# Kernel optimization log

Measured on AMD Instinct MI355X. Metric: run time of the kernel, lower is better.

## Reference

```python
import jax, jax.numpy as jnp
import numpy as np

B, IN, MEM, CTX, H = 8192, 1024, 1024, 1024, 4
DH = CTX // H

def setup_inputs() -> dict:
    key = jax.random.key(0)
    ks = jax.random.split(key, 20)
    s = 0.02
    d = {
        'input_tensor': jax.random.normal(ks[0], (B, IN), jnp.float32),
        'previous_memory': jax.random.normal(ks[1], (B, MEM), jnp.float32),
        # MultiheadAttention packed in_proj (q,k,v) and out_proj
        'in_proj_w': jax.random.normal(ks[2], (3 * CTX, CTX), jnp.float32) * s,
        'in_proj_b': jnp.zeros((3 * CTX,), jnp.float32),
        'out_proj_w': jax.random.normal(ks[3], (CTX, CTX), jnp.float32) * s,
        'out_proj_b': jnp.zeros((CTX,), jnp.float32),
        # input/memory projections
        'ip_w': jax.random.normal(ks[4], (CTX, IN), jnp.float32) * s,
        'ip_b': jnp.zeros((CTX,), jnp.float32),
        'mp_w': jax.random.normal(ks[5], (CTX, MEM), jnp.float32) * s,
        'mp_b': jnp.zeros((CTX,), jnp.float32),
        # forget / output gates
        'fg_w': jax.random.normal(ks[6], (MEM, MEM + IN), jnp.float32) * s,
        'fg_b': jnp.zeros((MEM,), jnp.float32),
        'og_w': jax.random.normal(ks[7], (MEM, MEM), jnp.float32) * s,
        'og_b': jnp.zeros((MEM,), jnp.float32),
        # GRUCell weights (PyTorch layout: [3*hidden, in], gates order r,z,n)
        'gru_w_ih': jax.random.normal(ks[8], (3 * MEM, CTX), jnp.float32) * s,
        'gru_b_ih': jnp.zeros((3 * MEM,), jnp.float32),
        'gru_w_hh': jax.random.normal(ks[9], (3 * MEM, MEM), jnp.float32) * s,
        'gru_b_hh': jnp.zeros((3 * MEM,), jnp.float32),
    }
    return d

def _forward(input_tensor, previous_memory, in_proj_w, in_proj_b, out_proj_w, out_proj_b,
             ip_w, ip_b, mp_w, mp_b, fg_w, fg_b, og_w, og_b,
             gru_w_ih, gru_b_ih, gru_w_hh, gru_b_hh):
    # projections
    pi = input_tensor @ ip_w.T + ip_b          # [B, CTX] (query; also context/value)
    pm = previous_memory @ mp_w.T + mp_b       # [B, CTX] (key)
    # MHA with q_len = kv_len = 1: softmax over a single key -> weights = 1
    wq, wk, wv = jnp.split(in_proj_w, 3, axis=0)
    bq, bk, bv = jnp.split(in_proj_b, 3, axis=0)
    q = (pi @ wq.T + bq).reshape(B, H, DH)
    k = (pm @ wk.T + bk).reshape(B, H, DH)
    v = (pi @ wv.T + bv).reshape(B, H, DH)
    scores = jnp.sum(q * k, axis=-1, keepdims=True) / jnp.sqrt(jnp.float32(DH))  # [B,H,1]
    w = jax.nn.softmax(scores, axis=-1)        # all ones (single key)
    attn = (w * v).reshape(B, CTX)             # == v
    context_aware = attn @ out_proj_w.T + out_proj_b  # [B, CTX]
    attention_weights = jnp.mean(w, axis=1)[:, None, :]  # [B,1,1], avg over heads
    # forget gate
    forget_in = jnp.concatenate([previous_memory, input_tensor], axis=-1)
    fgate = jax.nn.sigmoid(forget_in @ fg_w.T + fg_b)
    gated_mem = previous_memory * fgate
    # GRUCell (PyTorch semantics)
    gi = context_aware @ gru_w_ih.T + gru_b_ih
    gh = gated_mem @ gru_w_hh.T + gru_b_hh
    gi_r, gi_z, gi_n = jnp.split(gi, 3, axis=-1)
    gh_r, gh_z, gh_n = jnp.split(gh, 3, axis=-1)
    r = jax.nn.sigmoid(gi_r + gh_r)
    z = jax.nn.sigmoid(gi_z + gh_z)
    n = jnp.tanh(gi_n + r * gh_n)
    updated = (1.0 - z) * n + z * gated_mem
    ogate = jax.nn.sigmoid(updated @ og_w.T + og_b)
    return updated * ogate, attention_weights

def reference(input_tensor, previous_memory, in_proj_w, in_proj_b, out_proj_w, out_proj_b,
              ip_w, ip_b, mp_w, mp_b, fg_w, fg_b, og_w, og_b,
              gru_w_ih, gru_b_ih, gru_w_hh, gru_b_hh):
    return _forward(input_tensor, previous_memory, in_proj_w, in_proj_b, out_proj_w, out_proj_b,
                    ip_w, ip_b, mp_w, mp_b, fg_w, fg_b, og_w, og_b,
                    gru_w_ih, gru_b_ih, gru_w_hh, gru_b_hh)
```

## Files before the change

### kernel.cpp

```cpp
#include <hip/hip_runtime.h>
#include <cstdint>
#include <cstddef>


typedef __bf16 bf16;
typedef bf16 bf16x4 __attribute__((ext_vector_type(4)));
typedef bf16 bf16x8 __attribute__((ext_vector_type(8)));
typedef float f32x4 __attribute__((ext_vector_type(4)));

#define B_ROWS 8192

__device__ __forceinline__ float sigmoid_f(float x) {
    return 1.0f / (1.0f + __expf(-x));
}
__device__ __forceinline__ float tanh_f(float x) {
    return 1.0f - 2.0f / (__expf(2.0f * x) + 1.0f);
}

template <int BM>
__device__ __forceinline__ void gemm_core_tb(
    bf16* sA, bf16* sB,
    const bf16* __restrict__ A, int lda,
    const bf16* __restrict__ W, int ldw,
    const float* __restrict__ bias,
    int N, int K, int brow, int bcol, int epi,
    bf16* __restrict__ out_bf, float* __restrict__ out_f32,
    const float* __restrict__ aux_f32, const bf16* __restrict__ aux_bf,
    int tld)
{
    constexpr int AI = BM / 32;
    const int tid  = threadIdx.x;
    const int lane = tid & 63;
    const int wave = tid >> 6;
    const int wr   = (wave & 1) * (BM / 2);
    const int wc   = (wave >> 1) * 64;
    const int lrow = lane & 15;
    const int lq   = lane >> 4;

    f32x4 acc[AI][4];
#pragma unroll
    for (int i = 0; i < AI; ++i)
#pragma unroll
        for (int j = 0; j < 4; ++j) {
            f32x4 z = {0.0f, 0.0f, 0.0f, 0.0f};
            acc[i][j] = z;
        }

    auto stage = [&](bf16* dA, bf16* dB, int k0) {
#pragma unroll
        for (int i = 0; i < BM / 64; ++i) {
            const int s   = tid + i * 256;
            const int row = s >> 2;
            const int col = (((s & 3) ^ ((s >> 3) & 3)) << 3);
            const bf16* gp = A + (size_t)(brow + row) * lda + (k0 + col);
            __builtin_amdgcn_global_load_lds(
                (const __attribute__((address_space(1))) void*)gp,
                (__attribute__((address_space(3))) void*)(&dA[s * 8]),
                16, 0, 0);
        }
#pragma unroll
        for (int i = 0; i < 2; ++i) {
            const int s   = tid + i * 256;
            const int row = s >> 2;
            const int col = (((s & 3) ^ ((s >> 3) & 3)) << 3);
            const bf16* gp = W + (size_t)(bcol + row) * ldw + (k0 + col);
            __builtin_amdgcn_global_load_lds(
                (const __attribute__((address_space(1))) void*)gp,
                (__attribute__((address_space(3))) void*)(&dB[s * 8]),
                16, 0, 0);
        }
    };

#define WAIT_LPS()                                                   \
    do {                                                             \
        if constexpr (BM == 128)                                     \
            asm volatile("s_waitcnt vmcnt(4)" ::: "memory");         \
        else                                                         \
            asm volatile("s_waitcnt vmcnt(3)" ::: "memory");         \
    } while (0)

    const int NT = K >> 5;

    bf16* a0 = sA;               bf16* b0 = sB;
    bf16* a1 = sA + BM * 32;     bf16* b1 = sB + 4096;
    bf16* a2 = sA + 2 * BM * 32; bf16* b2 = sB + 2 * 4096;

    stage(a0, b0, 0);
    stage(a1, b1, NT > 1 ? 32 : 0);
    WAIT_LPS();
    __builtin_amdgcn_s_barrier();
    __builtin_amdgcn_sched_barrier(0);

    for (int kt = 0; kt < NT; ++kt) {
        bf16x8 av[AI], bv[4];
#pragma unroll
        for (int i = 0; i < AI; ++i) {
            const int r = wr + i * 16 + lrow;
            av[i] = *(const bf16x8*)&a0[r * 32 + ((lq ^ ((r >> 1) & 3)) << 3)];
        }
#pragma unroll
        for (int j = 0; j < 4; ++j) {
            const int r = wc + j * 16 + lrow;
            bv[j] = *(const bf16x8*)&b0[r * 32 + ((lq ^ ((r >> 1) & 3)) << 3)];
        }

        const int kn = (kt + 2 < NT ? kt + 2 : NT - 1) << 5;
        stage(a2, b2, kn);

#pragma unroll
        for (int i = 0; i < AI; ++i)
#pragma unroll
            for (int j = 0; j < 4; ++j)
                acc[i][j] = __builtin_amdgcn_mfma_f32_16x16x32_bf16(
                    av[i], bv[j], acc[i][j], 0, 0, 0);

        __builtin_amdgcn_sched_barrier(0);
        WAIT_LPS();
        __builtin_amdgcn_s_barrier();
        __builtin_amdgcn_sched_barrier(0);

        bf16* ta = a0; a0 = a1; a1 = a2; a2 = ta;
        bf16* tb = b0; b0 = b1; b1 = b2; b2 = tb;
    }

    asm volatile("s_waitcnt vmcnt(0)" ::: "memory");
#undef WAIT_LPS

#pragma unroll
    for (int j = 0; j < 4; ++j) {
        const int gcol = bcol + wc + j * 16 + lrow;
        const float bj = bias ? bias[gcol] : 0.0f;
#pragma unroll
        for (int i = 0; i < AI; ++i) {
            const int growb = brow + wr + i * 16 + lq * 4;
#pragma unroll
            for (int r = 0; r < 4; ++r) {
                const int grow = growb + r;
                const float val = acc[i][j][r] + bj;
                if (epi == 0) {
                    out_bf[(size_t)grow * N + gcol] = (bf16)val;
                } else if (epi == 1) {
                    const size_t idx = (size_t)grow * N + gcol;
                    out_bf[idx] = (bf16)(aux_f32[idx] * sigmoid_f(val));
                } else if (epi == 2) {
                    const size_t idx = (size_t)grow * N + gcol;
                    out_f32[idx] = (float)aux_bf[idx] * sigmoid_f(val);
                } else {
                    out_bf[(size_t)gcol * tld + grow] = (bf16)val;
                }
            }
        }
    }
}

__global__ __launch_bounds__(256, 2) void gemm128_k(
    const bf16* __restrict__ A, int lda, const bf16* __restrict__ W, int ldw,
    const float* __restrict__ bias, int N, int K, int epi,
    bf16* __restrict__ out_bf, float* __restrict__ out_f32,
    const float* __restrict__ aux_f32, const bf16* __restrict__ aux_bf,
    int tld, int nby)
{
    __shared__ bf16 sA[3 * 128 * 32];
    __shared__ bf16 sB[3 * 128 * 32];
    const int by = blockIdx.x % nby;
    const int bx = blockIdx.x / nby;
    gemm_core_tb<128>(sA, sB, A, lda, W, ldw, bias, N, K,
                      by * 128, bx * 128, epi,
                      out_bf, out_f32, aux_f32, aux_bf, tld);
}

__global__ __launch_bounds__(256, 2) void gemm64_k(
    const bf16* __restrict__ A, int lda, const bf16* __restrict__ W, int ldw,
    const float* __restrict__ bias, int N, int K, int epi,
    bf16* __restrict__ out_bf, float* __restrict__ out_f32,
    const float* __restrict__ aux_f32, const bf16* __restrict__ aux_bf,
    int tld, int nby)
{
    __shared__ bf16 sA[3 * 64 * 32];
    __shared__ bf16 sB[3 * 128 * 32];
    const int by = blockIdx.x % nby;
    const int bx = blockIdx.x / nby;
    gemm_core_tb<64>(sA, sB, A, lda, W, ldw, bias, N, K,
                     by * 64, bx * 128, epi,
                     out_bf, out_f32, aux_f32, aux_bf, tld);
}


__global__ void cast_weights_k(
    const float* __restrict__ wv, const float* __restrict__ wop,
    const float* __restrict__ wih, const float* __restrict__ wfg,
    const float* __restrict__ wog,
    bf16* __restrict__ dv, bf16* __restrict__ dop, bf16* __restrict__ dih,
    bf16* __restrict__ dfg, bf16* __restrict__ dog)
{
    int c = blockIdx.x * 256 + threadIdx.x;
    const float* s;
    bf16* d;
    int o;
    if (c < 262144)        { s = wv;  d = dv;  o = c; }
    else if (c < 524288)   { s = wop; d = dop; o = c - 262144; }
    else if (c < 1310720)  { s = wih; d = dih; o = c - 524288; }
    else if (c < 1835008)  { s = wfg; d = dfg; o = c - 1310720; }
    else                   { s = wog; d = dog; o = c - 1835008; }
    f32x4 v = ((const f32x4*)s)[o];
    bf16x4 t = {(bf16)v[0], (bf16)v[1], (bf16)v[2], (bf16)v[3]};
    ((bf16x4*)d)[o] = t;
}

__global__ void cast_f32_bf16_k(const float* __restrict__ src,
                                bf16* __restrict__ dst, int n4) {
    int i = blockIdx.x * 256 + threadIdx.x;
    if (i >= n4) return;
    f32x4 v = ((const f32x4*)src)[i];
    bf16x4 o = {(bf16)v[0], (bf16)v[1], (bf16)v[2], (bf16)v[3]};
    ((bf16x4*)dst)[i] = o;
}

__global__ void build_cat_k(const float* __restrict__ mem,
                            const float* __restrict__ inp,
                            bf16* __restrict__ cat) {
    int i = blockIdx.x * 256 + threadIdx.x;
    int row = i >> 9;
    int c4  = i & 511;
    f32x4 v;
    if (c4 < 256)
        v = ((const f32x4*)mem)[(size_t)row * 256 + c4];
    else
        v = ((const f32x4*)inp)[(size_t)row * 256 + (c4 - 256)];
    bf16x4 o = {(bf16)v[0], (bf16)v[1], (bf16)v[2], (bf16)v[3]};
    ((bf16x4*)cat)[i] = o;
}

__global__ void transpose_cast_k(const float* __restrict__ src,
                                 bf16* __restrict__ dst, int R, int C) {
    __shared__ float t[32][33];
    int bx = blockIdx.x * 32;
    int by = blockIdx.y * 32;
    int tx = threadIdx.x & 31, ty = threadIdx.x >> 5;
#pragma unroll
    for (int i = 0; i < 32; i += 8)
        t[ty + i][tx] = src[(size_t)(by + ty + i) * C + bx + tx];
    __syncthreads();
#pragma unroll
    for (int i = 0; i < 32; i += 8)
        dst[(size_t)(bx + ty + i) * R + by + tx] = (bf16)t[tx][ty + i];
}

__global__ void gemv_k(const float* __restrict__ W, const float* __restrict__ x,
                       const float* __restrict__ b, float* __restrict__ y,
                       int K) {
    int n    = blockIdx.x * 4 + (threadIdx.x >> 6);
    int lane = threadIdx.x & 63;
    const float* row = W + (size_t)n * K;
    float s = 0.0f;
    for (int k = lane * 4; k < K; k += 256) {
        f32x4 w = *(const f32x4*)(row + k);
        f32x4 xv = *(const f32x4*)(x + k);
        s += w[0] * xv[0] + w[1] * xv[1] + w[2] * xv[2] + w[3] * xv[3];
    }
#pragma unroll
    for (int off = 32; off; off >>= 1) s += __shfl_down(s, off);
    if (lane == 0) y[n] = s + b[n];
}

__global__ void gru_combine_k(const bf16* __restrict__ gi,
                              const bf16* __restrict__ gh,
                              bf16* __restrict__ gated) {
    int i   = blockIdx.x * 256 + threadIdx.x;
    int row = i >> 7;
    int c   = (i & 127) << 3;
    size_t b3 = (size_t)row * 3072 + c;
    size_t b1 = (size_t)row * 1024 + c;
    bf16x8 gir = *(const bf16x8*)(gi + b3);
    bf16x8 giz = *(const bf16x8*)(gi + b3 + 1024);
    bf16x8 gin = *(const bf16x8*)(gi + b3 + 2048);
    bf16x8 ghr = *(const bf16x8*)(gh + b3);
    bf16x8 ghz = *(const bf16x8*)(gh + b3 + 1024);
    bf16x8 ghn = *(const bf16x8*)(gh + b3 + 2048);
    bf16x8 g   = *(const bf16x8*)(gated + b1);
    bf16x8 o;
#pragma unroll
    for (int e = 0; e < 8; ++e) {
        float r = sigmoid_f((float)gir[e] + (float)ghr[e]);
        float z = sigmoid_f((float)giz[e] + (float)ghz[e]);
        float n = tanh_f((float)gin[e] + r * (float)ghn[e]);
        o[e] = (bf16)((1.0f - z) * n + z * (float)g[e]);
    }
    *(bf16x8*)(gated + b1) = o;
}

__global__ void fill_ones_k(float* __restrict__ p, int n) {
    int i = blockIdx.x * 256 + threadIdx.x;
    if (i < n) p[i] = 1.0f;
}

extern "C" void kernel_launch(void* const* d_in, const int* in_sizes, int n_in,
                              void* d_out, int out_size, void* d_ws,
                              size_t ws_size, hipStream_t stream) {
    const float* input      = (const float*)d_in[0];
    const float* prev       = (const float*)d_in[1];
    const float* in_proj_w  = (const float*)d_in[2];
    const float* in_proj_b  = (const float*)d_in[3];
    const float* out_proj_w = (const float*)d_in[4];
    const float* out_proj_b = (const float*)d_in[5];
    const float* ip_w       = (const float*)d_in[6];
    const float* ip_b       = (const float*)d_in[7];
    const float* fg_w  = (const float*)d_in[10];
    const float* fg_b  = (const float*)d_in[11];
    const float* og_w  = (const float*)d_in[12];
    const float* og_b  = (const float*)d_in[13];
    const float* gih_w = (const float*)d_in[14];
    const float* gih_b = (const float*)d_in[15];
    const float* ghh_w = (const float*)d_in[16];
    const float* ghh_b = (const float*)d_in[17];
    float* out = (float*)d_out;

    char* ws = (char*)d_ws;
    const size_t MB = 1024 * 1024;
    bf16* CAT   = (bf16*)(ws);
    bf16* WHHB  = (bf16*)(ws);
    bf16* GI    = (bf16*)(ws + 32 * MB);
    bf16* GH    = (bf16*)(ws + 80 * MB);
    bf16* WVB   = (bf16*)(ws + 80 * MB);
    bf16* WOPB  = (bf16*)(ws + 82 * MB);
    bf16* WIHB  = (bf16*)(ws + 84 * MB);
    bf16* WIPT  = (bf16*)(ws + 90 * MB);
    bf16* T1T   = (bf16*)(ws + 92 * MB);
    bf16* T2T   = (bf16*)(ws + 94 * MB);
    bf16* WFGB  = (bf16*)(ws + 96 * MB);
    float* T1B  = (float*)(ws + 100 * MB);
    float* T2B  = (float*)(ws + 100 * MB + 8192);
    float* T3B  = (float*)(ws + 100 * MB + 16384);
    bf16* GATED = (bf16*)(ws + 128 * MB);
    bf16* WCOMB = (bf16*)(ws + 144 * MB);
    bf16* WOGB  = (bf16*)(ws + 150 * MB);

    const int M = B_ROWS;
    dim3 blk(256);

    build_cat_k<<<dim3((M * 2048 / 4) / 256), blk, 0, stream>>>(prev, input, CAT);
    cast_weights_k<<<dim3(8192), blk, 0, stream>>>(
        in_proj_w + 2048 * 1024, out_proj_w, gih_w, fg_w, og_w,
        WVB, WOPB, WIHB, WFGB, WOGB);
    transpose_cast_k<<<dim3(32, 32), blk, 0, stream>>>(ip_w, WIPT, 1024, 1024);
    gemv_k<<<dim3(256), blk, 0, stream>>>(in_proj_w + 2048 * 1024, ip_b, in_proj_b + 2048, T1B, 1024);
    gemv_k<<<dim3(256), blk, 0, stream>>>(out_proj_w, T1B, out_proj_b, T2B, 1024);
    gemv_k<<<dim3(768), blk, 0, stream>>>(gih_w, T2B, gih_b, T3B, 1024);
    gemm64_k<<<dim3(128), blk, 0, stream>>>(WVB, 1024, WIPT, 1024, nullptr,
        1024, 1024, 3, T1T, nullptr, nullptr, nullptr, 1024, 16);
    gemm64_k<<<dim3(128), blk, 0, stream>>>(WOPB, 1024, T1T, 1024, nullptr,
        1024, 1024, 3, T2T, nullptr, nullptr, nullptr, 1024, 16);
    gemm64_k<<<dim3(384), blk, 0, stream>>>(WIHB, 1024, T2T, 1024, nullptr,
        1024, 1024, 0, WCOMB, nullptr, nullptr, nullptr, 0, 48);
    gemm128_k<<<dim3(512), blk, 0, stream>>>(CAT, 2048, WFGB, 2048,
        fg_b, 1024, 2048, 1, GATED, nullptr, prev, nullptr, 0, 64);
    gemm128_k<<<dim3(1536), blk, 0, stream>>>(CAT + 1024, 2048, WCOMB,
        1024, T3B, 3072, 1024, 0, GI, nullptr, nullptr, nullptr, 0, 64);
    cast_f32_bf16_k<<<dim3(3072), blk, 0, stream>>>(ghh_w, WHHB, 3072 * 1024 / 4);
    gemm128_k<<<dim3(1536), blk, 0, stream>>>(GATED, 1024, WHHB, 1024,
        ghh_b, 3072, 1024, 0, GH, nullptr, nullptr, nullptr, 0, 64);
    gru_combine_k<<<dim3(M * 1024 / 8 / 256), blk, 0, stream>>>(GI, GH, GATED);
    gemm128_k<<<dim3(512), blk, 0, stream>>>(GATED, 1024, WOGB, 1024,
        og_b, 1024, 1024, 2, nullptr, out, nullptr, GATED, 0, 64);
    fill_ones_k<<<dim3(32), blk, 0, stream>>>(out + (size_t)M * 1024, M);
}
```

Baseline: 531.8 us.

## Add 256x128-tile triple-buffered GEMM kernel for the two large GRU projections

Introduces a new bf16 MFMA GEMM kernel with 256x128 output tiles, a three-stage LDS ring filled by direct global-to-LDS loads, XOR-swizzled LDS layout, and an LDS-staged coalesced bf16 epilogue with bias. It replaces the 128-tile GEMM for the GI and GH projections (8192x3072x1024), halving the block count and raising per-block arithmetic intensity to cut global/LDS traffic per FLOP. The larger tile uses 128 accumulator registers per thread and about 72KB LDS, which may limit occupancy, and the kernel assumes dimensions divisible by the tile sizes.

```diff
diff --git a/kernel.cpp b/kernel.cpp
--- a/kernel.cpp
+++ b/kernel.cpp
@@ -15,6 +15,132 @@
 }
 __device__ __forceinline__ float tanh_f(float x) {
     return 1.0f - 2.0f / (__expf(2.0f * x) + 1.0f);
+}
+
+__global__ __launch_bounds__(256, 2) void gemm256x128_k(
+    const bf16* __restrict__ A, int lda,
+    const bf16* __restrict__ W, int ldw,
+    const float* __restrict__ bias, int N, int K,
+    bf16* __restrict__ out_bf, int nby)
+{
+    __shared__ bf16 lds[36864];
+    bf16* sA = lds;
+    bf16* sB = lds + 3 * 256 * 32;
+
+    const int tid  = threadIdx.x;
+    const int lane = tid & 63;
+    const int wave = tid >> 6;
+    const int wm   = wave >> 1;
+    const int wn   = wave & 1;
+    const int lrow = lane & 15;
+    const int lq   = lane >> 4;
+
+    const int by   = blockIdx.x % nby;
+    const int bx   = blockIdx.x / nby;
+    const int brow = by * 256;
+    const int bcol = bx * 128;
+
+    f32x4 acc[8][4];
+#pragma unroll
+    for (int i = 0; i < 8; ++i)
+#pragma unroll
+        for (int j = 0; j < 4; ++j) {
+            f32x4 z = {0.0f, 0.0f, 0.0f, 0.0f};
+            acc[i][j] = z;
+        }
+
+    auto stage = [&](bf16* dA, bf16* dB, int k0) {
+#pragma unroll
+        for (int i = 0; i < 4; ++i) {
+            const int s   = tid + i * 256;
+            const int row = s >> 2;
+            const int col = (((s & 3) ^ ((s >> 3) & 3)) << 3);
+            const bf16* gp = A + (size_t)(brow + row) * lda + (k0 + col);
+            __builtin_amdgcn_global_load_lds(
+                (const __attribute__((address_space(1))) void*)gp,
+                (__attribute__((address_space(3))) void*)(&dA[s * 8]),
+                16, 0, 0);
+        }
+#pragma unroll
+        for (int i = 0; i < 2; ++i) {
+            const int s   = tid + i * 256;
+            const int row = s >> 2;
+            const int col = (((s & 3) ^ ((s >> 3) & 3)) << 3);
+            const bf16* gp = W + (size_t)(bcol + row) * ldw + (k0 + col);
+            __builtin_amdgcn_global_load_lds(
+                (const __attribute__((address_space(1))) void*)gp,
+                (__attribute__((address_space(3))) void*)(&dB[s * 8]),
+                16, 0, 0);
+        }
+    };
+
+    const int NT = K >> 5;
+
+    bf16* a0 = sA;                bf16* b0 = sB;
+    bf16* a1 = sA + 256 * 32;     bf16* b1 = sB + 128 * 32;
+    bf16* a2 = sA + 2 * 256 * 32; bf16* b2 = sB + 2 * 128 * 32;
+
+    stage(a0, b0, 0);
+    stage(a1, b1, 32);
+    asm volatile("s_waitcnt vmcnt(6)" ::: "memory");
+    __builtin_amdgcn_s_barrier();
+    __builtin_amdgcn_sched_barrier(0);
+
+    for (int kt = 0; kt < NT; ++kt) {
+        bf16x8 av[8], bv[4];
+#pragma unroll
+        for (int i = 0; i < 8; ++i) {
+            const int r = wm * 128 + i * 16 + lrow;
+            av[i] = *(const bf16x8*)&a0[r * 32 + ((lq ^ ((r >> 1) & 3)) << 3)];
+        }
+#pragma unroll
+        for (int j = 0; j < 4; ++j) {
+            const int r = wn * 64 + j * 16 + lrow;
+            bv[j] = *(const bf16x8*)&b0[r * 32 + ((lq ^ ((r >> 1) & 3)) << 3)];
+        }
+
+        const int kn = (kt + 2 < NT ? kt + 2 : NT - 1) << 5;
+        stage(a2, b2, kn);
+
+#pragma unroll
+        for (int i = 0; i < 8; ++i)
+#pragma unroll
+            for (int j = 0; j < 4; ++j)
+                acc[i][j] = __builtin_amdgcn_mfma_f32_16x16x32_bf16(
+                    av[i], bv[j], acc[i][j], 0, 0, 0);
+
+        __builtin_amdgcn_sched_barrier(0);
+        asm volatile("s_waitcnt vmcnt(6)" ::: "memory");
+        __builtin_amdgcn_s_barrier();
+        __builtin_amdgcn_sched_barrier(0);
+
+        bf16* ta = a0; a0 = a1; a1 = a2; a2 = ta;
+        bf16* tb = b0; b0 = b1; b1 = b2; b2 = tb;
+    }
+
+    asm volatile("s_waitcnt vmcnt(0)" ::: "memory");
+
+    bf16* cb = lds;
+#pragma unroll
+    for (int j = 0; j < 4; ++j) {
+        const int col = wn * 64 + j * 16 + lrow;
+        const float bj = bias[bcol + col];
+#pragma unroll
+        for (int i = 0; i < 8; ++i) {
+            const int rowb = wm * 128 + i * 16 + lq * 4;
+#pragma unroll
+            for (int r = 0; r < 4; ++r)
+                cb[(rowb + r) * 136 + col] = (bf16)(acc[i][j][r] + bj);
+        }
+    }
+    __syncthreads();
+#pragma unroll
+    for (int p = 0; p < 16; ++p) {
+        const int row = p * 16 + (tid >> 4);
+        const int col = (tid & 15) * 8;
+        bf16x8 v = *(const bf16x8*)&cb[row * 136 + col];
+        *(bf16x8*)&out_bf[(size_t)(brow + row) * N + bcol + col] = v;
+    }
 }
 
 template <int BM>
@@ -354,11 +480,11 @@
         1024, 1024, 0, WCOMB, nullptr, nullptr, nullptr, 0, 48);
     gemm128_k<<<dim3(512), blk, 0, stream>>>(CAT, 2048, WFGB, 2048,
         fg_b, 1024, 2048, 1, GATED, nullptr, prev, nullptr, 0, 64);
-    gemm128_k<<<dim3(1536), blk, 0, stream>>>(CAT + 1024, 2048, WCOMB,
-        1024, T3B, 3072, 1024, 0, GI, nullptr, nullptr, nullptr, 0, 64);
+    gemm256x128_k<<<dim3(768), blk, 0, stream>>>(CAT + 1024, 2048, WCOMB,
+        1024, T3B, 3072, 1024, GI, 32);
     cast_f32_bf16_k<<<dim3(3072), blk, 0, stream>>>(ghh_w, WHHB, 3072 * 1024 / 4);
-    gemm128_k<<<dim3(1536), blk, 0, stream>>>(GATED, 1024, WHHB, 1024,
-        ghh_b, 3072, 1024, 0, GH, nullptr, nullptr, nullptr, 0, 64);
+    gemm256x128_k<<<dim3(768), blk, 0, stream>>>(GATED, 1024, WHHB,
+        1024, ghh_b, 3072, 1024, GH, 32);
     gru_combine_k<<<dim3(M * 1024 / 8 / 256), blk, 0, stream>>>(GI, GH, GATED);
     gemm128_k<<<dim3(512), blk, 0, stream>>>(GATED, 1024, WOGB, 1024,
         og_b, 1024, 1024, 2, nullptr, out, nullptr, GATED, 0, 64);
```

New measurement: 491.1 us. 1.08x faster.
